# Kernel tuning notes

Measured on AMD Instinct MI355X. Metric: run time of the kernel, lower is better.

Reference implementation:

```python
import jax, jax.numpy as jnp
import numpy as np

PATCH = 14
MERGE = 2
HIDDEN = 1024
# (H, W) in pixels; all multiples of PATCH with even patch grids (divisible by MERGE)
IMAGE_SIZES = np.array([[1540, 1540], [1120, 1540], [1540, 896], [784, 1260],
                        [1512, 1512], [1540, 1120], [896, 896], [1260, 1540]], dtype=np.int64)


def setup_inputs() -> dict:
    key = jax.random.key(0)
    k1, k2 = jax.random.split(key)
    sizes_p = IMAGE_SIZES // PATCH
    total_tokens = int((sizes_p[:, 0] * sizes_p[:, 1]).sum())  # 67440
    image_features = jax.random.normal(k1, (total_tokens, HIDDEN), dtype=jnp.float32)
    # nn.Linear(hidden*merge**2 -> hidden, bias=False): weight shape [out, in] = [1024, 4096]
    merging_weight = jax.random.normal(k2, (HIDDEN, HIDDEN * MERGE * MERGE), dtype=jnp.float32) * 0.02
    image_sizes = jnp.asarray(IMAGE_SIZES)
    return {"image_features": image_features, "merging_weight": merging_weight, "image_sizes": image_sizes}


def _merge_patches(feats, sizes_np):
    """Per-image unfold(kernel=MERGE, stride=MERGE) over the [hp, wp] patch grid.
    torch unfold orders the flattened channel dim as d*m*m + ki*m + kj (channel-major),
    blocks in row-major (i, j) order -> reshape/transpose below reproduces it exactly."""
    m = MERGE
    D = feats.shape[-1]
    out, off = [], 0
    for h, w in sizes_np:  # small fixed set of images (static shapes)
        hp, wp = int(h) // PATCH, int(w) // PATCH
        n = hp * wp
        g = jax.lax.dynamic_slice_in_dim(feats, off, n, axis=0)
        g = g.reshape(hp // m, m, wp // m, m, D)          # [i, ki, j, kj, d]
        g = g.transpose(0, 2, 4, 1, 3).reshape(-1, D * m * m)  # [i*j, d*ki*kj]
        out.append(g)
        off += n
    return jnp.concatenate(out, axis=0)  # [total_tokens / m^2, D*m^2]


def reference(image_features, merging_weight, image_sizes):
    sizes_np = np.asarray(jax.device_get(image_sizes))  # static metadata
    merged = _merge_patches(image_features, sizes_np)
    return merged @ merging_weight.T  # [total/4, HIDDEN]
```

## Files before the change

### kernel.cpp

```cpp
#include <hip/hip_runtime.h>
#include <hip/hip_bf16.h>

#define MTOK  16860
#define NTOK  67440
#define NOUT  1024
#define KDIM  4096
#define NBM   132
#define KTILES 64

__device__ __constant__ int c_mend[8] = {3025,5225,6985,8245,11161,13361,14385,16860};
__device__ __constant__ int c_moff[8] = {0,3025,5225,6985,8245,11161,13361,14385};
__device__ __constant__ int c_foff[8] = {0,12100,20900,27940,32980,44644,53444,57540};
__device__ __constant__ int c_wp[8]   = {110,110,64,90,108,80,64,110};

typedef __attribute__((ext_vector_type(8))) short          bf16x8;
typedef __attribute__((ext_vector_type(8))) unsigned short u16x8;
typedef __attribute__((ext_vector_type(4))) float          f32x4;

__device__ __forceinline__ unsigned short f2bf(float f) {
    unsigned int u = __float_as_uint(f);
    u += 0x7FFFu + ((u >> 16) & 1u);
    return (unsigned short)(u >> 16);
}

__device__ __forceinline__ void async_copy16(const void* g, void* l) {
    __builtin_amdgcn_global_load_lds(
        (const __attribute__((address_space(1))) void*)g,
        (__attribute__((address_space(3))) void*)l, 16, 0, 0);
}

#define CF_BLOCKS 33720
__global__ __launch_bounds__(256) void cast_all(const float* __restrict__ feats,
                                                const float* __restrict__ W,
                                                unsigned short* __restrict__ fb,
                                                unsigned short* __restrict__ Wb) {
    int b = blockIdx.x;
    if (b < CF_BLOCKS) {
        size_t g = ((size_t)b * 256 + threadIdx.x) * 8;
        float4 a = *(const float4*)(feats + g);
        float4 c = *(const float4*)(feats + g + 4);
        u16x8 v;
        v[0]=f2bf(a.x); v[1]=f2bf(a.y); v[2]=f2bf(a.z); v[3]=f2bf(a.w);
        v[4]=f2bf(c.x); v[5]=f2bf(c.y); v[6]=f2bf(c.z); v[7]=f2bf(c.w);
        *(u16x8*)(fb + g) = v;
    } else {
        int g = (b - CF_BLOCKS) * 256 + threadIdx.x;
        int n = g >> 10, d = g & 1023;
        float4 v = *(const float4*)(W + (size_t)n * 4096 + d * 4);
        unsigned short* o = Wb + (size_t)n * 4096 + d;
        o[0]    = f2bf(v.x);
        o[1024] = f2bf(v.y);
        o[2048] = f2bf(v.z);
        o[3072] = f2bf(v.w);
    }
}

__global__ __launch_bounds__(256, 2) void gemm_fused(const unsigned short* __restrict__ A,
                                                     const unsigned short* __restrict__ B,
                                                     float* __restrict__ C) {
    __shared__ unsigned short lA[2][128 * 64];
    __shared__ unsigned short lB[2][128 * 64];

    const int orig    = blockIdx.y * 8 + blockIdx.x;
    const int logical = (orig & 7) * NBM + (orig >> 3);
    const int bn = logical & 7;
    const int bm = logical >> 3;

    const int tid  = threadIdx.x;
    const int wave = tid >> 6, lane = tid & 63;
    const int wm = (wave >> 1) * 64, wn = (wave & 1) * 64;

    const int srow = tid >> 3;
    const int sp   = tid & 7;
    const int ssw  = (sp ^ (srow & 7)) * 8;
    const int sdst = srow * 64 + sp * 8;

    int fbase[4], fwp[4];
#pragma unroll
    for (int i = 0; i < 4; ++i) {
        int t = bm * 128 + i * 32 + srow;
        if (t >= MTOK) t = 0;
        int im = 0;
        while (t >= c_mend[im]) im++;
        int rr  = t - c_moff[im];
        int wp  = c_wp[im];
        int wp2 = wp >> 1;
        int ii = rr / wp2, jj = rr - ii * wp2;
        fbase[i] = c_foff[im] + 2 * ii * wp + 2 * jj;
        fwp[i]   = wp;
    }
    const unsigned short* Bb = B + (size_t)(bn * 128) * KDIM;

    auto stage = [&](int kt, int buf) {
        const int k0 = kt * 64;
        const int c  = k0 >> 10;
        const int dA = (k0 & 1023) + ssw;
#pragma unroll
        for (int i = 0; i < 4; ++i) {
            int fr = fbase[i] + ((c & 2) ? fwp[i] : 0) + (c & 1);
            async_copy16(A + (((size_t)fr) << 10) + dA, &lA[buf][i * 2048 + sdst]);
        }
#pragma unroll
        for (int i = 0; i < 4; ++i) {
            async_copy16(Bb + (size_t)(i * 32 + srow) * KDIM + k0 + ssw,
                         &lB[buf][i * 2048 + sdst]);
        }
    };

    f32x4 acc[4][4];
#pragma unroll
    for (int a = 0; a < 4; ++a)
#pragma unroll
        for (int b = 0; b < 4; ++b) acc[a][b] = (f32x4){0.f, 0.f, 0.f, 0.f};

    const int mrow = lane & 15;
    const int q8   = (lane >> 4) * 8;
    const int rsw  = (mrow & 7) * 8;

    stage(0, 0);
    stage(1, 1);

#pragma unroll 2
    for (int kt = 0; kt < KTILES; ++kt) {
        const int cur = kt & 1;
        if (kt < KTILES - 1) {
            asm volatile("s_waitcnt vmcnt(8)" ::: "memory");
        } else {
            asm volatile("s_waitcnt vmcnt(0)" ::: "memory");
        }
        __builtin_amdgcn_s_barrier();
        __builtin_amdgcn_sched_barrier(0);

        bf16x8 af[2][4], bfr[2][4];
#pragma unroll
        for (int ks = 0; ks < 2; ++ks) {
            const int col = (ks * 32 + q8) ^ rsw;
#pragma unroll
            for (int a = 0; a < 4; ++a) {
                af[ks][a]  = *(const bf16x8*)&lA[cur][(wm + a * 16 + mrow) * 64 + col];
                bfr[ks][a] = *(const bf16x8*)&lB[cur][(wn + a * 16 + mrow) * 64 + col];
            }
        }
        __builtin_amdgcn_s_setprio(1);
#pragma unroll
        for (int ks = 0; ks < 2; ++ks)
#pragma unroll
            for (int a = 0; a < 4; ++a)
#pragma unroll
                for (int b = 0; b < 4; ++b)
                    acc[a][b] = __builtin_amdgcn_mfma_f32_16x16x32_bf16(af[ks][a], bfr[ks][b],
                                                                        acc[a][b], 0, 0, 0);
        __builtin_amdgcn_s_setprio(0);
        __builtin_amdgcn_sched_barrier(0);
        __builtin_amdgcn_s_barrier();
        if (kt + 2 < KTILES) stage(kt + 2, cur);
    }

    const int col   = lane & 15;
    const int rquad = (lane >> 4) * 4;
#pragma unroll
    for (int a = 0; a < 4; ++a) {
        int gm0 = bm * 128 + wm + a * 16 + rquad;
#pragma unroll
        for (int b = 0; b < 4; ++b) {
            int gn = bn * 128 + wn + b * 16 + col;
#pragma unroll
            for (int rg = 0; rg < 4; ++rg) {
                int gm = gm0 + rg;
                if (gm < MTOK) C[(size_t)gm * NOUT + gn] = acc[a][b][rg];
            }
        }
    }
}

__global__ __launch_bounds__(256) void naive_fb(const float* __restrict__ feats,
                                                const float* __restrict__ W,
                                                float* __restrict__ out) {
    int t = blockIdx.x;
    int o = blockIdx.y * 256 + threadIdx.x;
    int im = 0;
    while (t >= c_mend[im]) im++;
    int r = t - c_moff[im];
    int wp = c_wp[im], wp2 = wp >> 1;
    int i = r / wp2, j = r - i * wp2;
    const float* f00 = feats + (size_t)(c_foff[im] + (2*i)*wp + 2*j) * 1024;
    const float* f10 = f00 + (size_t)wp * 1024;
    const float* w = W + (size_t)o * 4096;
    float s = 0.f;
    for (int d = 0; d < 1024; ++d)
        s += f00[d] * w[d*4] + f00[d+1024] * w[d*4+1] + f10[d] * w[d*4+2] + f10[d+1024] * w[d*4+3];
    out[(size_t)t * 1024 + o] = s;
}

extern "C" void kernel_launch(void* const* d_in, const int* in_sizes, int n_in,
                              void* d_out, int out_size, void* d_ws, size_t ws_size,
                              hipStream_t stream) {
    const float* feats = (const float*)d_in[0];
    const float* W     = (const float*)d_in[1];
    float* out         = (float*)d_out;

    const size_t need = ((size_t)NTOK * 1024 + (size_t)NOUT * KDIM) * sizeof(unsigned short);
    if (ws_size >= need) {
        unsigned short* featsbf = (unsigned short*)d_ws;
        unsigned short* Wb      = featsbf + (size_t)NTOK * 1024;
        cast_all<<<dim3(CF_BLOCKS + 4096), 256, 0, stream>>>(feats, W, featsbf, Wb);
        gemm_fused<<<dim3(NOUT / 128, NBM), 256, 0, stream>>>(featsbf, Wb, out);
    } else {
        naive_fb<<<dim3(MTOK, 4), 256, 0, stream>>>(feats, W, out);
    }
}
```

Measured before the change: 611.3 us.

## Fuse fp32-to-bf16 feature cast into GEMM via register-staged A loads

Drops the separate pass that converted all image features to bf16. The GEMM now reads fp32 features directly into registers, converts them with packed bf16 instructions and writes them to swizzled LDS, while B still streams through async global-to-LDS copies. The main loop is restructured into a two-stage register/LDS pipeline with explicit vmcnt waits. This removes the 276MB fp32 read plus bf16 write-and-reread of the cast kernel, but it doubles A-operand global traffic inside the GEMM (each A row is re-read by all 8 N-blocks in fp32) and raises register pressure.

Measured after the change: 604.3 us. Within noise of the previous version (-1.2%).

```diff
diff --git a/kernel.cpp b/kernel.cpp
--- a/kernel.cpp
+++ b/kernel.cpp
@@ -17,47 +17,42 @@
 typedef __attribute__((ext_vector_type(8))) unsigned short u16x8;
 typedef __attribute__((ext_vector_type(4))) float          f32x4;
 
+#define VMCNT(n) asm volatile("s_waitcnt vmcnt(" #n ")" ::: "memory")
+#define LGKM0()  asm volatile("s_waitcnt lgkmcnt(0)" ::: "memory")
+
 __device__ __forceinline__ unsigned short f2bf(float f) {
     unsigned int u = __float_as_uint(f);
     u += 0x7FFFu + ((u >> 16) & 1u);
     return (unsigned short)(u >> 16);
 }
 
+__device__ __forceinline__ unsigned int pkbf(float lo, float hi) {
+    unsigned int r;
+    asm("v_cvt_pk_bf16_f32 %0, %1, %2" : "=v"(r) : "v"(lo), "v"(hi));
+    return r;
+}
+
 __device__ __forceinline__ void async_copy16(const void* g, void* l) {
     __builtin_amdgcn_global_load_lds(
         (const __attribute__((address_space(1))) void*)g,
         (__attribute__((address_space(3))) void*)l, 16, 0, 0);
 }
 
-#define CF_BLOCKS 33720
-__global__ __launch_bounds__(256) void cast_all(const float* __restrict__ feats,
-                                                const float* __restrict__ W,
-                                                unsigned short* __restrict__ fb,
-                                                unsigned short* __restrict__ Wb) {
-    int b = blockIdx.x;
-    if (b < CF_BLOCKS) {
-        size_t g = ((size_t)b * 256 + threadIdx.x) * 8;
-        float4 a = *(const float4*)(feats + g);
-        float4 c = *(const float4*)(feats + g + 4);
-        u16x8 v;
-        v[0]=f2bf(a.x); v[1]=f2bf(a.y); v[2]=f2bf(a.z); v[3]=f2bf(a.w);
-        v[4]=f2bf(c.x); v[5]=f2bf(c.y); v[6]=f2bf(c.z); v[7]=f2bf(c.w);
-        *(u16x8*)(fb + g) = v;
-    } else {
-        int g = (b - CF_BLOCKS) * 256 + threadIdx.x;
-        int n = g >> 10, d = g & 1023;
-        float4 v = *(const float4*)(W + (size_t)n * 4096 + d * 4);
-        unsigned short* o = Wb + (size_t)n * 4096 + d;
-        o[0]    = f2bf(v.x);
-        o[1024] = f2bf(v.y);
-        o[2048] = f2bf(v.z);
-        o[3072] = f2bf(v.w);
-    }
-}
-
-__global__ __launch_bounds__(256, 2) void gemm_fused(const unsigned short* __restrict__ A,
-                                                     const unsigned short* __restrict__ B,
-                                                     float* __restrict__ C) {
+__global__ __launch_bounds__(256) void cast_w_perm(const float* __restrict__ W,
+                                                   unsigned short* __restrict__ Wb) {
+    int g = blockIdx.x * 256 + threadIdx.x;
+    int n = g >> 10, d = g & 1023;
+    float4 v = *(const float4*)(W + (size_t)n * 4096 + d * 4);
+    unsigned short* o = Wb + (size_t)n * 4096 + d;
+    o[0]    = f2bf(v.x);
+    o[1024] = f2bf(v.y);
+    o[2048] = f2bf(v.z);
+    o[3072] = f2bf(v.w);
+}
+
+__global__ __launch_bounds__(256, 2) void gemm_direct(const float* __restrict__ F,
+                                                      const unsigned short* __restrict__ B,
+                                                      float* __restrict__ C) {
     __shared__ unsigned short lA[2][128 * 64];
     __shared__ unsigned short lB[2][128 * 64];
 
@@ -72,7 +67,8 @@
 
     const int srow = tid >> 3;
     const int sp   = tid & 7;
-    const int ssw  = (sp ^ (srow & 7)) * 8;
+    const int sw   = srow & 7;
+    const int bssw = (sp ^ sw) * 8;
     const int sdst = srow * 64 + sp * 8;
 
     int fbase[4], fwp[4];
@@ -91,20 +87,34 @@
     }
     const unsigned short* Bb = B + (size_t)(bn * 128) * KDIM;
 
-    auto stage = [&](int kt, int buf) {
-        const int k0 = kt * 64;
+    auto issueA = [&](int t, float4* rg) {
+        const int k0 = t * 64;
         const int c  = k0 >> 10;
-        const int dA = (k0 & 1023) + ssw;
+        const int dA = (k0 & 1023) + sp * 8;
 #pragma unroll
         for (int i = 0; i < 4; ++i) {
             int fr = fbase[i] + ((c & 2) ? fwp[i] : 0) + (c & 1);
-            async_copy16(A + (((size_t)fr) << 10) + dA, &lA[buf][i * 2048 + sdst]);
-        }
+            const float* src = F + (((size_t)fr) << 10) + dA;
+            rg[2 * i]     = *(const float4*)(src);
+            rg[2 * i + 1] = *(const float4*)(src + 4);
+        }
+    };
+    auto writeA = [&](float4* rg, int buf) {
 #pragma unroll
         for (int i = 0; i < 4; ++i) {
-            async_copy16(Bb + (size_t)(i * 32 + srow) * KDIM + k0 + ssw,
+            float4 x = rg[2 * i], y = rg[2 * i + 1];
+            uint4 v;
+            v.x = pkbf(x.x, x.y); v.y = pkbf(x.z, x.w);
+            v.z = pkbf(y.x, y.y); v.w = pkbf(y.z, y.w);
+            *(uint4*)&lA[buf][(i * 32 + srow) * 64 + ((sp ^ sw) * 8)] = v;
+        }
+    };
+    auto issueB = [&](int t, int buf) {
+        const int k0 = t * 64;
+#pragma unroll
+        for (int i = 0; i < 4; ++i)
+            async_copy16(Bb + (size_t)(i * 32 + srow) * KDIM + k0 + bssw,
                          &lB[buf][i * 2048 + sdst]);
-        }
     };
 
     f32x4 acc[4][4];
@@ -117,20 +127,7 @@
     const int q8   = (lane >> 4) * 8;
     const int rsw  = (mrow & 7) * 8;
 
-    stage(0, 0);
-    stage(1, 1);
-
-#pragma unroll 2
-    for (int kt = 0; kt < KTILES; ++kt) {
-        const int cur = kt & 1;
-        if (kt < KTILES - 1) {
-            asm volatile("s_waitcnt vmcnt(8)" ::: "memory");
-        } else {
-            asm volatile("s_waitcnt vmcnt(0)" ::: "memory");
-        }
-        __builtin_amdgcn_s_barrier();
-        __builtin_amdgcn_sched_barrier(0);
-
+    auto frag_mfma = [&](int cur) {
         bf16x8 af[2][4], bfr[2][4];
 #pragma unroll
         for (int ks = 0; ks < 2; ++ks) {
@@ -151,10 +148,52 @@
                     acc[a][b] = __builtin_amdgcn_mfma_f32_16x16x32_bf16(af[ks][a], bfr[ks][b],
                                                                         acc[a][b], 0, 0, 0);
         __builtin_amdgcn_s_setprio(0);
+    };
+
+    float4 r1[8], r2[8];
+
+    issueA(0, r1);
+    issueB(0, 0);
+    VMCNT(4);
+    writeA(r1, 0);
+    issueA(1, r2);
+    VMCNT(8);
+    LGKM0();
+    __builtin_amdgcn_sched_barrier(0);
+    __builtin_amdgcn_s_barrier();
+    issueB(1, 1);
+
+#pragma unroll 1
+    for (int kt = 0; kt < 62; kt += 2) {
+        frag_mfma(0);
+        VMCNT(4);
+        writeA(r2, 1);
+        issueA(kt + 2, r1);
+        VMCNT(8);
+        LGKM0();
         __builtin_amdgcn_sched_barrier(0);
         __builtin_amdgcn_s_barrier();
-        if (kt + 2 < KTILES) stage(kt + 2, cur);
-    }
+        issueB(kt + 2, 0);
+
+        frag_mfma(1);
+        VMCNT(4);
+        writeA(r1, 0);
+        issueA(kt + 3, r2);
+        VMCNT(8);
+        LGKM0();
+        __builtin_amdgcn_sched_barrier(0);
+        __builtin_amdgcn_s_barrier();
+        issueB(kt + 3, 1);
+    }
+
+    frag_mfma(0);
+    VMCNT(4);
+    writeA(r2, 1);
+    VMCNT(0);
+    LGKM0();
+    __builtin_amdgcn_sched_barrier(0);
+    __builtin_amdgcn_s_barrier();
+    frag_mfma(1);
 
     const int col   = lane & 15;
     const int rquad = (lane >> 4) * 4;
@@ -199,12 +238,11 @@
     const float* W     = (const float*)d_in[1];
     float* out         = (float*)d_out;
 
-    const size_t need = ((size_t)NTOK * 1024 + (size_t)NOUT * KDIM) * sizeof(unsigned short);
+    const size_t need = (size_t)NOUT * KDIM * sizeof(unsigned short);
     if (ws_size >= need) {
-        unsigned short* featsbf = (unsigned short*)d_ws;
-        unsigned short* Wb      = featsbf + (size_t)NTOK * 1024;
-        cast_all<<<dim3(CF_BLOCKS + 4096), 256, 0, stream>>>(feats, W, featsbf, Wb);
-        gemm_fused<<<dim3(NOUT / 128, NBM), 256, 0, stream>>>(featsbf, Wb, out);
+        unsigned short* Wb = (unsigned short*)d_ws;
+        cast_w_perm<<<dim3(4096), 256, 0, stream>>>(W, Wb);
+        gemm_direct<<<dim3(8, NBM), 256, 0, stream>>>(feats, Wb, out);
     } else {
         naive_fb<<<dim3(MTOK, 4), 256, 0, stream>>>(feats, W, out);
     }
```
